# Kernel tuning notes

Hardware: AMD Instinct MI355X
Metric: run time of the kernel (lower is better)

Reference implementation:

```python
import jax, jax.numpy as jnp
import numpy as np

G = 512      # graphs per batch
PER = 800    # nodes per graph
N = G * PER  # total nodes
X = 256      # x_size (= h_size so layers compose)
H = 256      # h_size
VOCAB = 32000
NCLS = 104


def setup_inputs() -> dict:
    rng = np.random.default_rng(0)
    # Random tree per graph: node 0 is root, parent(i) uniform in [0, i)
    i_idx = np.arange(1, PER)
    parents = np.floor(rng.random((G, PER - 1)) * i_idx).astype(np.int64)
    base = (np.arange(G) * PER)[:, None]
    edge_dst = (parents + base).reshape(-1)                     # parent (message receiver)
    edge_src = (np.tile(np.arange(1, PER), (G, 1)) + base).reshape(-1)  # child
    E = edge_src.size
    child_count = np.bincount(edge_dst, minlength=N)
    # sort edges by (dst, src) so child position = rank among siblings
    order = np.lexsort((edge_src, edge_dst))
    edge_src = edge_src[order]
    edge_dst = edge_dst[order]
    starts = np.cumsum(child_count) - child_count
    pos = np.arange(E) - starts[edge_dst]
    n = child_count[edge_dst]
    # position-dependent interpolation coefficient: n==1 -> (W_l+W_r)/2 i.e. alpha=0.5
    alpha = np.where(n == 1, 0.5, pos / np.maximum(n - 1, 1)).astype(np.float32)

    node_type = rng.integers(0, VOCAB, N).astype(np.int32)
    graph_ids = np.repeat(np.arange(G), PER).astype(np.int32)

    key = jax.random.key(0)
    ks = jax.random.split(key, 6)
    s = 0.05
    emb = jax.random.normal(ks[0], (VOCAB, X), jnp.float32) * s
    W_left = jax.random.normal(ks[1], (X, H), jnp.float32) * s
    W_right = jax.random.normal(ks[2], (X, H), jnp.float32) * s
    W_top = jax.random.normal(ks[3], (X, H), jnp.float32) * s
    b_conv = jnp.zeros((H,), jnp.float32)
    gate_w = jax.random.normal(ks[4], (H, 1), jnp.float32) * s
    gate_b = jnp.zeros((1,), jnp.float32)
    cls_w = jax.random.normal(ks[5], (H, NCLS), jnp.float32) * s
    cls_b = jnp.zeros((NCLS,), jnp.float32)

    return dict(
        node_type=jnp.asarray(node_type), edge_src=jnp.asarray(edge_src.astype(np.int32)),
        edge_dst=jnp.asarray(edge_dst.astype(np.int32)), alpha=jnp.asarray(alpha),
        child_count=jnp.asarray(child_count.astype(np.int32)), graph_ids=jnp.asarray(graph_ids),
        emb=emb, W_left=W_left, W_right=W_right, W_top=W_top, b_conv=b_conv,
        gate_w=gate_w, gate_b=gate_b, cls_w=cls_w, cls_b=cls_b,
    )


def reference(node_type, edge_src, edge_dst, alpha, child_count, graph_ids,
              emb, W_left, W_right, W_top, b_conv,
              gate_w, gate_b, cls_w, cls_b):
    h = emb[node_type]                                  # [N, X]
    # TBCNN conv layer: sum_i ((1-a_i) W_left + a_i W_right) h_child_i
    #                 = (sum (1-a_i) h_i) W_left + (sum a_i h_i) W_right
    h_src = h[edge_src]                                 # [E, X]
    left = jax.ops.segment_sum(h_src * (1.0 - alpha)[:, None], edge_dst, num_segments=N)
    right = jax.ops.segment_sum(h_src * alpha[:, None], edge_dst, num_segments=N)
    conv = jax.nn.relu(left @ W_left + right @ W_right + h @ W_top + b_conv)
    # nodes without children receive no message -> keep embedding (DGL semantics)
    h = jnp.where((child_count > 0)[:, None], conv, h)  # [N, H]

    # GlobalAttentionPooling: per-graph softmax over gate scores
    gate = h @ gate_w + gate_b                          # [N, 1]
    gmax = jax.ops.segment_max(gate, graph_ids, num_segments=G)
    e = jnp.exp(gate - gmax[graph_ids])
    denom = jax.ops.segment_sum(e, graph_ids, num_segments=G)
    attn = e / denom[graph_ids]                         # [N, 1]
    pooled = jax.ops.segment_sum(h * attn, graph_ids, num_segments=G)  # [G, H]

    return pooled @ cls_w + cls_b                       # [G, NCLS]
```

## Files before the change

### kernel.cpp

```cpp
#include <hip/hip_runtime.h>
#include <stdint.h>

#define XH   256
#define NCLS 104

typedef _Float16 half2v __attribute__((ext_vector_type(2)));
typedef _Float16 half4v __attribute__((ext_vector_type(4)));
typedef _Float16 half8v __attribute__((ext_vector_type(8)));
typedef __attribute__((ext_vector_type(4))) float floatx4;

__device__ __forceinline__ void gll16(const void* g, void* l) {
    __builtin_amdgcn_global_load_lds(
        (const __attribute__((address_space(1))) unsigned*)g,
        (__attribute__((address_space(3))) unsigned*)l, 16, 0, 0);
}

__device__ __forceinline__ float fdot2f(half2v a, half2v b, float c) {
#if __has_builtin(__builtin_amdgcn_fdot2)
    return __builtin_amdgcn_fdot2(a, b, c, false);
#else
    return c + (float)a[0] * (float)b[0] + (float)a[1] * (float)b[1];
#endif
}

__global__ __launch_bounds__(256)
void k_prep(const float* __restrict__ Wl, const float* __restrict__ Wr,
            const float* __restrict__ Wt, _Float16* __restrict__ Btw) {
    int idx = blockIdx.x * 256 + threadIdx.x;
    if (idx >= 3 * XH * XH) return;
    int n = idx >> 8, k = idx & 255;
    int m, c;
    if (n < 512) { m = n & 1; c = n >> 1; }
    else         { m = 2;     c = n - 512; }
    const float* W = (m == 0) ? Wl : (m == 1) ? Wr : Wt;
    Btw[idx] = (_Float16)W[k * XH + c];
}

__global__ __launch_bounds__(256)
void k_gemm(const float* __restrict__ emb, const _Float16* __restrict__ Btw,
            const float* __restrict__ b_conv,
            const int* __restrict__ edge_src, const int* __restrict__ edge_dst,
            const float* __restrict__ alpha, const int* __restrict__ node_type,
            _Float16* __restrict__ Ylr, _Float16* __restrict__ Yt,
            _Float16* __restrict__ embf, int2* __restrict__ epk,
            int* __restrict__ row_start, int Mb, int E) {
    __shared__ __align__(16) _Float16 Ab[128 * 32];
    __shared__ __align__(16) _Float16 Bb[128 * 32];

    const int bx  = blockIdx.x;
    const int tid = threadIdx.x;

    if (bx >= Mb * 6) {
        int e = (bx - Mb * 6) * 256 + tid;
        if (e < E) {
            int s = edge_src[e];
            float a = alpha[e];
            half2v w = { (_Float16)(1.f - a), (_Float16)a };
            int2 p;
            p.x = node_type[s] * 512;
            p.y = __builtin_bit_cast(int, w);
            epk[e] = p;
            int d = edge_dst[e];
            if (e == 0 || edge_dst[e - 1] != d) row_start[d] = e;
        }
        return;
    }

    const int m0   = (bx / 6) * 128;
    const int ng   = bx % 6;
    const int n0   = ng * 128;
    const int lane = tid & 63;
    const int wv   = tid >> 6;
    const int mw   = wv >> 1;
    const int nw   = wv & 1;
    const int quad = lane >> 4;
    const int l15  = lane & 15;

    floatx4 acc[4][4];
    #pragma unroll
    for (int i = 0; i < 4; i++)
        #pragma unroll
        for (int j = 0; j < 4; j++) acc[i][j] = floatx4{0.f, 0.f, 0.f, 0.f};

    const int ar = tid >> 1;
    const int ah = (tid & 1) * 16;
    const int lq = lane >> 2;
    const int lb = (lane & 3) * 16;

    for (int kc = 0; kc < 8; kc++) {
        #pragma unroll
        for (int i = 0; i < 2; i++) {
            int issue = wv * 2 + i;
            int row   = issue * 16 + lq;
            gll16((const char*)Btw + (size_t)(n0 + row) * 512 + kc * 64 + lb,
                  (char*)Bb + issue * 1024);
        }
        {
            const float* ga = &emb[(size_t)(m0 + ar) * XH + kc * 32 + ah];
            floatx4 f0 = *(const floatx4*)ga;
            floatx4 f1 = *(const floatx4*)(ga + 4);
            floatx4 f2 = *(const floatx4*)(ga + 8);
            floatx4 f3 = *(const floatx4*)(ga + 12);
            half8v h0, h1;
            #pragma unroll
            for (int i = 0; i < 4; i++) {
                h0[i]     = (_Float16)f0[i];
                h0[4 + i] = (_Float16)f1[i];
                h1[i]     = (_Float16)f2[i];
                h1[4 + i] = (_Float16)f3[i];
            }
            *(half8v*)&Ab[ar * 32 + ah]     = h0;
            *(half8v*)&Ab[ar * 32 + ah + 8] = h1;
            if (ng == 0) {
                _Float16* ep = &embf[(size_t)(m0 + ar) * XH + kc * 32 + ah];
                *(half8v*)ep       = h0;
                *(half8v*)(ep + 8) = h1;
            }
        }
        __syncthreads();
        half8v a[4];
        #pragma unroll
        for (int mt = 0; mt < 4; mt++)
            a[mt] = *(const half8v*)&Ab[(mw * 64 + mt * 16 + l15) * 32 + quad * 8];
        #pragma unroll
        for (int nt = 0; nt < 4; nt++) {
            half8v b = *(const half8v*)&Bb[(nw * 64 + nt * 16 + l15) * 32 + quad * 8];
            #pragma unroll
            for (int mt = 0; mt < 4; mt++)
                acc[mt][nt] = __builtin_amdgcn_mfma_f32_16x16x32_f16(a[mt], b, acc[mt][nt], 0, 0, 0);
        }
        __syncthreads();
    }

    const bool isT = (n0 >= 512);
    #pragma unroll
    for (int nt = 0; nt < 4; nt++) {
        int col = n0 + nw * 64 + nt * 16 + l15;
        float bias = isT ? b_conv[col - 512] : 0.f;
        #pragma unroll
        for (int mt = 0; mt < 4; mt++) {
            #pragma unroll
            for (int r = 0; r < 4; r++) {
                int row = m0 + mw * 64 + mt * 16 + quad * 4 + r;
                _Float16 val = (_Float16)(acc[mt][nt][r] + bias);
                if (isT) Yt[(size_t)row * XH + (col - 512)] = val;
                else     Ylr[(size_t)row * 512 + col] = val;
            }
        }
    }
}

__global__ __launch_bounds__(1024, 8)
void k_graph(const int* __restrict__ node_type, const int* __restrict__ child_count,
             const _Float16* __restrict__ embf,
             const _Float16* __restrict__ Ylr, const _Float16* __restrict__ Yt,
             const int2* __restrict__ epk, const int* __restrict__ row_start,
             const float* __restrict__ gate_w, const float* __restrict__ gate_b,
             const float* __restrict__ cls_w, const float* __restrict__ cls_b,
             float* __restrict__ out, int PER) {
    const int g    = blockIdx.x;
    const int tid  = threadIdx.x;
    const int lane = tid & 63;
    const int wv   = tid >> 6;
    const int base = g * PER;

    __shared__ float pw[16 * XH];
    __shared__ float ds[16];
    __shared__ float pooled[XH];

    float gw4[4];
    #pragma unroll
    for (int i = 0; i < 4; i++) gw4[i] = gate_w[4 * lane + i];
    const float gb = gate_b[0];

    float acc4[4] = {0.f, 0.f, 0.f, 0.f};
    float dsum = 0.f;

    int vg = base + wv;
    int c  = child_count[vg];
    int tv = node_type[vg];
    int rs = row_start[vg];

    for (int v = wv; v < PER; v += 16) {
        int cn = 0, tvn = 0, rsn = 0;
        if (v + 16 < PER) {
            cn  = child_count[vg + 16];
            tvn = node_type[vg + 16];
            rsn = row_start[vg + 16];
        }

        float h4[4];
        if (c == 0) {
            half4v hv = *(const half4v*)&embf[(size_t)tv * XH + 4 * lane];
            #pragma unroll
            for (int i = 0; i < 4; i++) h4[i] = (float)hv[i];
        } else {
            half4v yt = *(const half4v*)&Yt[(size_t)tv * XH + 4 * lane];
            float s4[4] = {0.f, 0.f, 0.f, 0.f};
            int e = rs, e1 = rs + c;
            for (; e + 2 <= e1; e += 2) {
                int2 p0 = epk[e], p1 = epk[e + 1];
                half8v y0 = *(const half8v*)&Ylr[(size_t)p0.x + 8 * lane];
                half8v y1 = *(const half8v*)&Ylr[(size_t)p1.x + 8 * lane];
                half2v w0 = __builtin_bit_cast(half2v, p0.y);
                half2v w1 = __builtin_bit_cast(half2v, p1.y);
                #pragma unroll
                for (int i = 0; i < 4; i++)
                    s4[i] = fdot2f(half2v{y0[2 * i], y0[2 * i + 1]}, w0, s4[i]);
                #pragma unroll
                for (int i = 0; i < 4; i++)
                    s4[i] = fdot2f(half2v{y1[2 * i], y1[2 * i + 1]}, w1, s4[i]);
            }
            if (e < e1) {
                int2 p0 = epk[e];
                half8v y0 = *(const half8v*)&Ylr[(size_t)p0.x + 8 * lane];
                half2v w0 = __builtin_bit_cast(half2v, p0.y);
                #pragma unroll
                for (int i = 0; i < 4; i++)
                    s4[i] = fdot2f(half2v{y0[2 * i], y0[2 * i + 1]}, w0, s4[i]);
            }
            #pragma unroll
            for (int i = 0; i < 4; i++)
                h4[i] = fmaxf(s4[i] + (float)yt[i], 0.f);
        }

        float sg = h4[0] * gw4[0] + h4[1] * gw4[1] + h4[2] * gw4[2] + h4[3] * gw4[3];
        #pragma unroll
        for (int o = 1; o < 64; o <<= 1) sg += __shfl_xor(sg, o);
        float ew = __expf(sg + gb);
        dsum += ew;
        #pragma unroll
        for (int i = 0; i < 4; i++) acc4[i] += ew * h4[i];

        c = cn; tv = tvn; rs = rsn; vg += 16;
    }

    #pragma unroll
    for (int i = 0; i < 4; i++) pw[wv * XH + 4 * lane + i] = acc4[i];
    if (lane == 0) ds[wv] = dsum;
    __syncthreads();

    if (tid < XH) {
        float p = 0.f, d = 0.f;
        #pragma unroll
        for (int w = 0; w < 16; w++) p += pw[w * XH + tid];
        #pragma unroll
        for (int w = 0; w < 16; w++) d += ds[w];
        pooled[tid] = p / d;
    }
    __syncthreads();

    if (tid < NCLS) {
        float o = cls_b[tid];
        #pragma unroll 8
        for (int k = 0; k < XH; k++) o += pooled[k] * cls_w[k * NCLS + tid];
        out[g * NCLS + tid] = o;
    }
}

extern "C" void kernel_launch(void* const* d_in, const int* in_sizes, int n_in,
                              void* d_out, int out_size, void* d_ws, size_t ws_size,
                              hipStream_t stream) {
    const int*   node_type   = (const int*)d_in[0];
    const int*   edge_src    = (const int*)d_in[1];
    const int*   edge_dst    = (const int*)d_in[2];
    const float* alpha       = (const float*)d_in[3];
    const int*   child_count = (const int*)d_in[4];
    const float* emb         = (const float*)d_in[6];
    const float* Wl          = (const float*)d_in[7];
    const float* Wr          = (const float*)d_in[8];
    const float* Wt          = (const float*)d_in[9];
    const float* b_conv      = (const float*)d_in[10];
    const float* gate_w      = (const float*)d_in[11];
    const float* gate_b      = (const float*)d_in[12];
    const float* cls_w       = (const float*)d_in[13];
    const float* cls_b       = (const float*)d_in[14];

    const int N     = in_sizes[0];
    const int E     = in_sizes[1];
    const int vocab = in_sizes[6] / XH;
    const int G     = out_size / NCLS;
    const int PER   = N / G;
    const int Mb    = vocab / 128;
    const int Eb    = (E + 255) / 256;

    _Float16* Ylr  = (_Float16*)d_ws;
    _Float16* Yt   = Ylr + (size_t)vocab * 512;
    _Float16* embf = Yt + (size_t)vocab * XH;
    _Float16* Btw  = embf + (size_t)vocab * XH;
    int2*     epk  = (int2*)(Btw + 3 * XH * XH);
    int*      row_start = (int*)(epk + E);

    hipLaunchKernelGGL(k_prep, dim3((3 * XH * XH + 255) / 256), dim3(256), 0, stream,
                       Wl, Wr, Wt, Btw);

    hipLaunchKernelGGL(k_gemm, dim3(Mb * 6 + Eb), dim3(256), 0, stream,
                       emb, Btw, b_conv, edge_src, edge_dst, alpha, node_type,
                       Ylr, Yt, embf, epk, row_start, Mb, E);

    hipLaunchKernelGGL(k_graph, dim3(G), dim3(1024), 0, stream,
                       node_type, child_count, embf, Ylr, Yt, epk, row_start,
                       gate_w, gate_b, cls_w, cls_b, (float*)d_out, PER);
}
```

Baseline: 253.2 us.

## Restructure vocab GEMM with resident A tile and precompute alpha-specialized projection tables

```diff
diff --git a/kernel.cpp b/kernel.cpp
--- a/kernel.cpp
+++ b/kernel.cpp
@@ -14,7 +14,6 @@
         (const __attribute__((address_space(1))) unsigned*)g,
         (__attribute__((address_space(3))) unsigned*)l, 16, 0, 0);
 }
-
 __device__ __forceinline__ float fdot2f(half2v a, half2v b, float c) {
 #if __has_builtin(__builtin_amdgcn_fdot2)
     return __builtin_amdgcn_fdot2(a, b, c, false);
@@ -22,142 +21,154 @@
     return c + (float)a[0] * (float)b[0] + (float)a[1] * (float)b[1];
 #endif
 }
+__device__ __forceinline__ int MF(int x) { return (x + (x >> 2)) & 3; }
+
 
 __global__ __launch_bounds__(256)
 void k_prep(const float* __restrict__ Wl, const float* __restrict__ Wr,
-            const float* __restrict__ Wt, _Float16* __restrict__ Btw) {
-    int idx = blockIdx.x * 256 + threadIdx.x;
-    if (idx >= 3 * XH * XH) return;
-    int n = idx >> 8, k = idx & 255;
-    int m, c;
-    if (n < 512) { m = n & 1; c = n >> 1; }
-    else         { m = 2;     c = n - 512; }
-    const float* W = (m == 0) ? Wl : (m == 1) ? Wr : Wt;
-    Btw[idx] = (_Float16)W[k * XH + c];
-}
-
-__global__ __launch_bounds__(256)
-void k_gemm(const float* __restrict__ emb, const _Float16* __restrict__ Btw,
-            const float* __restrict__ b_conv,
+            const float* __restrict__ Wt,
             const int* __restrict__ edge_src, const int* __restrict__ edge_dst,
             const float* __restrict__ alpha, const int* __restrict__ node_type,
-            _Float16* __restrict__ Ylr, _Float16* __restrict__ Yt,
-            _Float16* __restrict__ embf, int2* __restrict__ epk,
-            int* __restrict__ row_start, int Mb, int E) {
-    __shared__ __align__(16) _Float16 Ab[128 * 32];
-    __shared__ __align__(16) _Float16 Bb[128 * 32];
-
-    const int bx  = blockIdx.x;
-    const int tid = threadIdx.x;
-
-    if (bx >= Mb * 6) {
-        int e = (bx - Mb * 6) * 256 + tid;
-        if (e < E) {
-            int s = edge_src[e];
-            float a = alpha[e];
-            half2v w = { (_Float16)(1.f - a), (_Float16)a };
-            int2 p;
-            p.x = node_type[s] * 512;
-            p.y = __builtin_bit_cast(int, w);
-            epk[e] = p;
-            int d = edge_dst[e];
-            if (e == 0 || edge_dst[e - 1] != d) row_start[d] = e;
-        }
+            _Float16* __restrict__ Btw, int2* __restrict__ epk,
+            int* __restrict__ row_start, int VQ, int E) {
+    int idx = blockIdx.x * 256 + threadIdx.x;
+    if (idx < 3 * XH * XH) {
+        int n = idx >> 8, k = idx & 255;
+        int m, c;
+        if (n < 512) { m = n & 1; c = n >> 1; }
+        else         { m = 2;     c = n - 512; }
+        const float* W = (m == 0) ? Wl : (m == 1) ? Wr : Wt;
+        Btw[idx] = (_Float16)W[k * XH + c];
         return;
     }
-
-    const int m0   = (bx / 6) * 128;
-    const int ng   = bx % 6;
-    const int n0   = ng * 128;
+    idx -= 3 * XH * XH;
+    if (idx < E) {
+        int s  = edge_src[idx];
+        float a = alpha[idx];
+        int ts = node_type[s];
+        int x;
+        if      (a == 0.0f) x = 2 * VQ + ts * 256;
+        else if (a == 1.0f) x = 3 * VQ + ts * 256;
+        else if (a == 0.5f) x = 4 * VQ + ts * 256;
+        else                x = (ts * 512) | 1;
+        half2v w = { (_Float16)(1.f - a), (_Float16)a };
+        int2 p;
+        p.x = x;
+        p.y = __builtin_bit_cast(int, w);
+        epk[idx] = p;
+        int d = edge_dst[idx];
+        if (idx == 0 || edge_dst[idx - 1] != d) row_start[d] = idx;
+    }
+}
+
+__global__ __launch_bounds__(512)
+void k_main(const float* __restrict__ emb, const _Float16* __restrict__ Btw,
+            const float* __restrict__ b_conv, _Float16* __restrict__ W16, int VQ) {
+    __shared__ __align__(16) _Float16 Ab[8][64][32];
+    __shared__ __align__(16) _Float16 Bb[2][128][32];
+
+    const int tid  = threadIdx.x;
     const int lane = tid & 63;
     const int wv   = tid >> 6;
-    const int mw   = wv >> 1;
-    const int nw   = wv & 1;
+    const int m0   = blockIdx.x * 64;
+    const int mw   = wv >> 2;
+    const int nw   = wv & 3;
     const int quad = lane >> 4;
     const int l15  = lane & 15;
 
-    floatx4 acc[4][4];
-    #pragma unroll
-    for (int i = 0; i < 4; i++)
-        #pragma unroll
-        for (int j = 0; j < 4; j++) acc[i][j] = floatx4{0.f, 0.f, 0.f, 0.f};
-
-    const int ar = tid >> 1;
-    const int ah = (tid & 1) * 16;
-    const int lq = lane >> 2;
-    const int lb = (lane & 3) * 16;
-
-    for (int kc = 0; kc < 8; kc++) {
-        #pragma unroll
-        for (int i = 0; i < 2; i++) {
-            int issue = wv * 2 + i;
-            int row   = issue * 16 + lq;
-            gll16((const char*)Btw + (size_t)(n0 + row) * 512 + kc * 64 + lb,
-                  (char*)Bb + issue * 1024);
-        }
-        {
-            const float* ga = &emb[(size_t)(m0 + ar) * XH + kc * 32 + ah];
+    {
+        const int kh  = tid >> 8;
+        const int u   = tid & 255;
+        const int row = u >> 2, rem = u & 3;
+        const int slot = rem ^ MF(row & 15);
+        #pragma unroll
+        for (int kc2 = 0; kc2 < 4; kc2++) {
+            int kc = kc2 * 2 + kh;
+            const float* ga = &emb[(size_t)(m0 + row) * XH + kc * 32 + rem * 8];
             floatx4 f0 = *(const floatx4*)ga;
             floatx4 f1 = *(const floatx4*)(ga + 4);
-            floatx4 f2 = *(const floatx4*)(ga + 8);
-            floatx4 f3 = *(const floatx4*)(ga + 12);
-            half8v h0, h1;
-            #pragma unroll
-            for (int i = 0; i < 4; i++) {
-                h0[i]     = (_Float16)f0[i];
-                h0[4 + i] = (_Float16)f1[i];
-                h1[i]     = (_Float16)f2[i];
-                h1[4 + i] = (_Float16)f3[i];
+            half8v h;
+            #pragma unroll
+            for (int i = 0; i < 4; i++) { h[i] = (_Float16)f0[i]; h[4 + i] = (_Float16)f1[i]; }
+            *(half8v*)&Ab[kc][row][slot * 8] = h;
+            *(half8v*)&W16[(size_t)6 * VQ + (size_t)(m0 + row) * XH + kc * 32 + rem * 8] = h;
+        }
+    }
+    const int brow = tid >> 2, pslot = tid & 3;
+    const int bd = pslot ^ MF(brow & 15);
+    gll16((const char*)Btw + (size_t)brow * 512 + bd * 16,
+          (char*)&Bb[0][0][0] + wv * 1024);
+    __syncthreads();
+
+    int buf = 0;
+    for (int ng = 0; ng < 6; ng++) {
+        floatx4 acc[2][2];
+        #pragma unroll
+        for (int i = 0; i < 2; i++)
+            #pragma unroll
+            for (int j = 0; j < 2; j++) acc[i][j] = floatx4{0.f, 0.f, 0.f, 0.f};
+
+        #pragma unroll
+        for (int kc = 0; kc < 8; kc++) {
+            int ni = ng * 8 + kc + 1;
+            if (ni < 48) {
+                int nng = ni >> 3, nkc = ni & 7;
+                gll16((const char*)Btw + (size_t)(nng * 128 + brow) * 512 + nkc * 64 + bd * 16,
+                      (char*)&Bb[buf ^ 1][0][0] + wv * 1024);
             }
-            *(half8v*)&Ab[ar * 32 + ah]     = h0;
-            *(half8v*)&Ab[ar * 32 + ah + 8] = h1;
-            if (ng == 0) {
-                _Float16* ep = &embf[(size_t)(m0 + ar) * XH + kc * 32 + ah];
-                *(half8v*)ep       = h0;
-                *(half8v*)(ep + 8) = h1;
+            half8v a[2], b[2];
+            #pragma unroll
+            for (int mt = 0; mt < 2; mt++)
+                a[mt] = *(const half8v*)&Ab[kc][mw * 32 + mt * 16 + l15][(quad ^ MF(l15)) * 8];
+            #pragma unroll
+            for (int nt = 0; nt < 2; nt++)
+                b[nt] = *(const half8v*)&Bb[buf][nw * 32 + nt * 16 + l15][(quad ^ MF(l15)) * 8];
+            #pragma unroll
+            for (int nt = 0; nt < 2; nt++)
+                #pragma unroll
+                for (int mt = 0; mt < 2; mt++)
+                    acc[mt][nt] = __builtin_amdgcn_mfma_f32_16x16x32_f16(a[mt], b[nt], acc[mt][nt], 0, 0, 0);
+            __syncthreads();
+            buf ^= 1;
+        }
+
+        const bool isT = (ng >= 4);
+        #pragma unroll
+        for (int nt = 0; nt < 2; nt++) {
+            int col = ng * 128 + nw * 32 + nt * 16 + l15;
+            float bias = isT ? b_conv[col - 512] : 0.f;
+            #pragma unroll
+            for (int mt = 0; mt < 2; mt++) {
+                #pragma unroll
+                for (int r = 0; r < 4; r++) {
+                    int row = m0 + mw * 32 + mt * 16 + quad * 4 + r;
+                    float v = acc[mt][nt][r] + bias;
+                    if (isT) {
+                        W16[(size_t)5 * VQ + (size_t)row * 256 + (col - 512)] = (_Float16)v;
+                    } else {
+                        W16[(size_t)row * 512 + col] = (_Float16)v;
+                        float pv = __shfl_xor(v, 1);
+                        int cp = col >> 1;
+                        if ((col & 1) == 0) {
+                            W16[(size_t)2 * VQ + (size_t)row * 256 + cp] = (_Float16)v;
+                            W16[(size_t)4 * VQ + (size_t)row * 256 + cp] = (_Float16)(0.5f * (v + pv));
+                        } else {
+                            W16[(size_t)3 * VQ + (size_t)row * 256 + cp] = (_Float16)v;
+                        }
+                    }
+                }
             }
         }
-        __syncthreads();
-        half8v a[4];
-        #pragma unroll
-        for (int mt = 0; mt < 4; mt++)
-            a[mt] = *(const half8v*)&Ab[(mw * 64 + mt * 16 + l15) * 32 + quad * 8];
-        #pragma unroll
-        for (int nt = 0; nt < 4; nt++) {
-            half8v b = *(const half8v*)&Bb[(nw * 64 + nt * 16 + l15) * 32 + quad * 8];
-            #pragma unroll
-            for (int mt = 0; mt < 4; mt++)
-                acc[mt][nt] = __builtin_amdgcn_mfma_f32_16x16x32_f16(a[mt], b, acc[mt][nt], 0, 0, 0);
-        }
-        __syncthreads();
-    }
-
-    const bool isT = (n0 >= 512);
-    #pragma unroll
-    for (int nt = 0; nt < 4; nt++) {
-        int col = n0 + nw * 64 + nt * 16 + l15;
-        float bias = isT ? b_conv[col - 512] : 0.f;
-        #pragma unroll
-        for (int mt = 0; mt < 4; mt++) {
-            #pragma unroll
-            for (int r = 0; r < 4; r++) {
-                int row = m0 + mw * 64 + mt * 16 + quad * 4 + r;
-                _Float16 val = (_Float16)(acc[mt][nt][r] + bias);
-                if (isT) Yt[(size_t)row * XH + (col - 512)] = val;
-                else     Ylr[(size_t)row * 512 + col] = val;
-            }
-        }
     }
 }
 
 __global__ __launch_bounds__(1024, 8)
-void k_graph(const int* __restrict__ node_type, const int* __restrict__ child_count,
-             const _Float16* __restrict__ embf,
-             const _Float16* __restrict__ Ylr, const _Float16* __restrict__ Yt,
+void k_graph(const int* __restrict__ nty, const int* __restrict__ cc,
+             const _Float16* __restrict__ W16,
              const int2* __restrict__ epk, const int* __restrict__ row_start,
              const float* __restrict__ gate_w, const float* __restrict__ gate_b,
              const float* __restrict__ cls_w, const float* __restrict__ cls_b,
-             float* __restrict__ out, int PER) {
+             float* __restrict__ out, int PER, int VQ) {
     const int g    = blockIdx.x;
     const int tid  = threadIdx.x;
     const int lane = tid & 63;
@@ -177,47 +188,44 @@
     float dsum = 0.f;
 
     int vg = base + wv;
-    int c  = child_count[vg];
-    int tv = node_type[vg];
-    int rs = row_start[vg];
+    int c  = cc[vg];
+    int tv = nty[vg];
+    int rs = (c > 0) ? row_start[vg] : 0;
+    half4v yt = *(const half4v*)&W16[(size_t)(c == 0 ? 6 : 5) * VQ + (size_t)tv * 256 + 4 * lane];
+    int2 pd0 = epk[rs];
 
     for (int v = wv; v < PER; v += 16) {
-        int cn = 0, tvn = 0, rsn = 0;
-        if (v + 16 < PER) {
-            cn  = child_count[vg + 16];
-            tvn = node_type[vg + 16];
-            rsn = row_start[vg + 16];
-        }
+        const bool has = (v + 16 < PER);
+        const int vns = has ? vg + 16 : vg;
+        int cn  = has ? cc[vns] : 0;
+        int tvn = nty[vns];
+        int rsn = (has && cn > 0) ? row_start[vns] : 0;
+        half4v ytn = *(const half4v*)&W16[(size_t)(cn == 0 ? 6 : 5) * VQ + (size_t)tvn * 256 + 4 * lane];
+        int2 pdn = epk[rsn];
 
         float h4[4];
         if (c == 0) {
-            half4v hv = *(const half4v*)&embf[(size_t)tv * XH + 4 * lane];
-            #pragma unroll
-            for (int i = 0; i < 4; i++) h4[i] = (float)hv[i];
+            #pragma unroll
+            for (int i = 0; i < 4; i++) h4[i] = (float)yt[i];
         } else {
-            half4v yt = *(const half4v*)&Yt[(size_t)tv * XH + 4 * lane];
             float s4[4] = {0.f, 0.f, 0.f, 0.f};
-            int e = rs, e1 = rs + c;
-            for (; e + 2 <= e1; e += 2) {
-                int2 p0 = epk[e], p1 = epk[e + 1];
-                half8v y0 = *(const half8v*)&Ylr[(size_t)p0.x + 8 * lane];
-                half8v y1 = *(const half8v*)&Ylr[(size_t)p1.x + 8 * lane];
-                half2v w0 = __builtin_bit_cast(half2v, p0.y);
-                half2v w1 = __builtin_bit_cast(half2v, p1.y);
-                #pragma unroll
-                for (int i = 0; i < 4; i++)
-                    s4[i] = fdot2f(half2v{y0[2 * i], y0[2 * i + 1]}, w0, s4[i]);
-                #pragma unroll
-                for (int i = 0; i < 4; i++)
-                    s4[i] = fdot2f(half2v{y1[2 * i], y1[2 * i + 1]}, w1, s4[i]);
-            }
-            if (e < e1) {
-                int2 p0 = epk[e];
-                half8v y0 = *(const half8v*)&Ylr[(size_t)p0.x + 8 * lane];
-                half2v w0 = __builtin_bit_cast(half2v, p0.y);
-                #pragma unroll
-                for (int i = 0; i < 4; i++)
-                    s4[i] = fdot2f(half2v{y0[2 * i], y0[2 * i + 1]}, w0, s4[i]);
+            int2 p = pd0;
+            int e = rs + 1;
+            const int e1 = rs + c;
+            while (true) {
+                if (p.x & 1) {
+                    half8v y = *(const half8v*)&W16[(size_t)(p.x ^ 1) + 8 * lane];
+                    half2v w = __builtin_bit_cast(half2v, p.y);
+                    #pragma unroll
+                    for (int i = 0; i < 4; i++)
+                        s4[i] = fdot2f(half2v{y[2 * i], y[2 * i + 1]}, w, s4[i]);
+                } else {
+                    half4v y = *(const half4v*)&W16[(size_t)p.x + 4 * lane];
+                    #pragma unroll
+                    for (int i = 0; i < 4; i++) s4[i] += (float)y[i];
+                }
+                if (e >= e1) break;
+                p = epk[e++];
             }
             #pragma unroll
             for (int i = 0; i < 4; i++)
@@ -232,7 +240,7 @@
         #pragma unroll
         for (int i = 0; i < 4; i++) acc4[i] += ew * h4[i];
 
-        c = cn; tv = tvn; rs = rsn; vg += 16;
+        c = cn; rs = rsn; yt = ytn; pd0 = pdn; vg = vns;
     }
 
     #pragma unroll
@@ -281,24 +289,21 @@
     const int vocab = in_sizes[6] / XH;
     const int G     = out_size / NCLS;
     const int PER   = N / G;
-    const int Mb    = vocab / 128;
-    const int Eb    = (E + 255) / 256;
-
-    _Float16* Ylr  = (_Float16*)d_ws;
-    _Float16* Yt   = Ylr + (size_t)vocab * 512;
-    _Float16* embf = Yt + (size_t)vocab * XH;
-    _Float16* Btw  = embf + (size_t)vocab * XH;
-    int2*     epk  = (int2*)(Btw + 3 * XH * XH);
+    const int VQ    = vocab * 256;
+
+    _Float16* W16 = (_Float16*)d_ws;
+    _Float16* Btw = W16 + (size_t)7 * VQ;
+    int2*     epk = (int2*)(Btw + 3 * XH * XH);
     int*      row_start = (int*)(epk + E);
 
-    hipLaunchKernelGGL(k_prep, dim3((3 * XH * XH + 255) / 256), dim3(256), 0, stream,
-                       Wl, Wr, Wt, Btw);
-
-    hipLaunchKernelGGL(k_gemm, dim3(Mb * 6 + Eb), dim3(256), 0, stream,
-                       emb, Btw, b_conv, edge_src, edge_dst, alpha, node_type,
-                       Ylr, Yt, embf, epk, row_start, Mb, E);
+    hipLaunchKernelGGL(k_prep, dim3((3 * XH * XH + E + 255) / 256), dim3(256), 0, stream,
+                       Wl, Wr, Wt, edge_src, edge_dst, alpha, node_type,
+                       Btw, epk, row_start, VQ, E);
+
+    hipLaunchKernelGGL(k_main, dim3(vocab / 64), dim3(512), 0, stream,
+                       emb, Btw, b_conv, W16, VQ);
 
     hipLaunchKernelGGL(k_graph, dim3(G), dim3(1024), 0, stream,
-                       node_type, child_count, embf, Ylr, Yt, epk, row_start,
-                       gate_w, gate_b, cls_w, cls_b, (float*)d_out, PER);
-}
+                       node_type, child_count, W16, epk, row_start,
+                       gate_w, gate_b, cls_w, cls_b, (float*)d_out, PER, VQ);
+}
```

Measured after the change: 250.0 us. No clear change (-1.2%).
